# Performance work log

Measured on AMD Instinct MI355X. Metric: run time of the kernel, lower is better.

The kernel has to match this reference:

```python
import jax, jax.numpy as jnp
import numpy as np
import math

DIM = 2048
B = 4
L = 4096
LOCAL_WINDOW = 512
GLOBAL_STRIDE = 1024
TOTAL_SEEN = 65536


def _sparse_cache_positions(total_seen):
    # Positions kept by _build_sparse_cache: local window tail + global strided.
    local_start = max(0, total_seen - LOCAL_WINDOW)
    glob = np.arange(0, local_start, GLOBAL_STRIDE)
    loc = np.arange(local_start, total_seen)
    return np.concatenate([glob, loc]).astype(np.int64)  # sorted, 576 entries


def setup_inputs() -> dict:
    key = jax.random.key(0)
    ks = jax.random.split(key, 12)
    pos = _sparse_cache_positions(TOTAL_SEEN)
    Kc = pos.shape[0]  # 576
    inp = {
        "chunk": jax.random.normal(ks[0], (B, L, DIM), dtype=jnp.float32),
        "cached_k": jax.random.normal(ks[1], (B, Kc, DIM), dtype=jnp.float32),
        "cached_v": jax.random.normal(ks[2], (B, Kc, DIM), dtype=jnp.float32),
        "cached_positions": jnp.asarray(pos),
        "total_seen": TOTAL_SEEN,
        "Wq": jax.random.normal(ks[3], (DIM, DIM), dtype=jnp.float32) * 0.02,
        "bq": jnp.zeros((DIM,), dtype=jnp.float32),
        "Wk": jax.random.normal(ks[4], (DIM, DIM), dtype=jnp.float32) * 0.02,
        "bk": jnp.zeros((DIM,), dtype=jnp.float32),
        "Wv": jax.random.normal(ks[5], (DIM, DIM), dtype=jnp.float32) * 0.02,
        "bv": jnp.zeros((DIM,), dtype=jnp.float32),
        "Wo": jax.random.normal(ks[6], (DIM, DIM), dtype=jnp.float32) * 0.02,
        "bo": jnp.zeros((DIM,), dtype=jnp.float32),
    }
    return inp


def reference(chunk, cached_k, cached_v, cached_positions, total_seen,
              Wq, bq, Wk, bk, Wv, bv, Wo, bo):
    Bn, Ln, D = chunk.shape
    scale = 1.0 / math.sqrt(D)
    # QKV projections (nn.Linear: x @ W.T + b)
    q = chunk @ Wq.T + bq            # [B, L, D]
    new_k = chunk @ Wk.T + bk        # [B, L, D]
    new_v = chunk @ Wv.T + bv
    new_pos = jnp.arange(total_seen, total_seen + Ln)  # [L]
    full_k = jnp.concatenate([cached_k, new_k], axis=1)   # [B, Kc+L, D]
    full_v = jnp.concatenate([cached_v, new_v], axis=1)
    full_pos = jnp.concatenate([cached_positions, new_pos], axis=0)  # [Kc+L]
    # Masked dense attention (causal on absolute positions)
    scores = jnp.einsum('bqd,bkd->bqk', q, full_k) * scale  # [B, L, Kc+L]
    causal = full_pos[None, :] > new_pos[:, None]           # [L, Kc+L]
    scores = jnp.where(causal[None, :, :], -jnp.inf, scores)
    weights = jax.nn.softmax(scores, axis=-1)
    attended = jnp.einsum('bqk,bkd->bqd', weights, full_v)  # [B, L, D]
    return attended @ Wo.T + bo
```

## Files before the change

### kernel.cpp

```cpp
#include <hip/hip_runtime.h>
#include <hip/hip_bf16.h>
#include <hip/hip_fp16.h>
#include <math.h>

#define B_   4
#define L_   4096
#define D_   2048
#define KC_  576
#define KT_  4672
#define KTP_ 4736

typedef __attribute__((ext_vector_type(8))) short short8;
typedef __attribute__((ext_vector_type(4))) float floatx4;

enum { EPI_BF16 = 0, EPI_KV = 1, EPI_SCORE = 2, EPI_F32 = 3 };
enum { FLAG_SWZ = 1, FLAG_KCAP = 2 };

__device__ static inline void gl_lds16(const void* g, void* l) {
  __builtin_amdgcn_global_load_lds((const __attribute__((address_space(1))) void*)g,
                                   (__attribute__((address_space(3))) void*)l,
                                   16, 0, 0);
}

__global__ __launch_bounds__(256) void gemm_bt(
    const ushort* __restrict__ A, int lda,
    const ushort* __restrict__ Bt, int ldb,
    void* __restrict__ out, int ldo,
    const float* __restrict__ bias,
    int K, int mode, int flags, float scale)
{
  __shared__ __align__(16) ushort As[128 * 32];
  __shared__ __align__(16) ushort Bs[128 * 32];
  const int t    = threadIdx.x;
  const int lane = t & 63;
  const int wave = t >> 6;

  int m_idx, n_idx;
  if (flags & FLAG_SWZ) {
    const int bid = blockIdx.x + (gridDim.x * blockIdx.y);
    n_idx = 2 * (bid & 7) + ((bid >> 3) & 1);
    m_idx = bid >> 4;
  } else {
    n_idx = blockIdx.x;
    m_idx = blockIdx.y;
  }
  const int bm = m_idx * 128;
  const int bn = n_idx * 128;

  if (mode == EPI_SCORE && bn >= KC_ + bm + 128) return;
  if (flags & FLAG_KCAP) {
    const int kcap = 704 + 128 * m_idx;
    if (K > kcap) K = kcap;
  }

  const int wm = (wave & 1) * 64;
  const int wn = (wave >> 1) * 64;

  floatx4 acc[4][4];
#pragma unroll
  for (int i = 0; i < 4; i++)
#pragma unroll
    for (int j = 0; j < 4; j++) acc[i][j] = (floatx4)(0.0f);

  const int srow = t >> 2;
  const int scol = (t & 3) * 8;
  const ushort* Ag = A  + (size_t)(bm + srow) * lda + scol;
  const ushort* Bg = Bt + (size_t)(bn + srow) * ldb + scol;
  char* AsB = (char*)As + wave * 1024;
  char* BsB = (char*)Bs + wave * 1024;
  const int fr = lane & 15;
  const int fq = lane >> 4;

  for (int k0 = 0; k0 < K; k0 += 32) {
    __syncthreads();
    gl_lds16(Ag + k0,                        AsB);
    gl_lds16(Ag + (size_t)64 * lda + k0,     AsB + 4096);
    gl_lds16(Bg + k0,                        BsB);
    gl_lds16(Bg + (size_t)64 * ldb + k0,     BsB + 4096);
    __syncthreads();

    short8 af[4], bf[4];
#pragma unroll
    for (int i = 0; i < 4; i++)
      af[i] = *(const short8*)(As + (wm + i * 16 + fr) * 32 + fq * 8);
#pragma unroll
    for (int j = 0; j < 4; j++)
      bf[j] = *(const short8*)(Bs + (wn + j * 16 + fr) * 32 + fq * 8);
#pragma unroll
    for (int i = 0; i < 4; i++)
#pragma unroll
      for (int j = 0; j < 4; j++)
        acc[i][j] = __builtin_amdgcn_mfma_f32_16x16x32_bf16(af[i], bf[j], acc[i][j], 0, 0, 0);
  }

#pragma unroll
  for (int i = 0; i < 4; i++) {
#pragma unroll
    for (int j = 0; j < 4; j++) {
      const int col = bn + wn + j * 16 + fr;
#pragma unroll
      for (int r = 0; r < 4; r++) {
        const int row = bm + wm + i * 16 + fq * 4 + r;
        float v = acc[i][j][r];
        if (mode == EPI_SCORE) {
          v *= scale;
          bool masked = (col >= KT_) || (col >= KC_ && (col - KC_) > row);
          if (masked) v = -65504.0f;
          ((__half*)out)[(size_t)row * ldo + col] = __float2half(v);
        } else if (mode == EPI_F32) {
          if (bias) v += bias[col];
          ((float*)out)[(size_t)row * ldo + col] = v;
        } else if (mode == EPI_KV) {
          if (bias) v += bias[col];
          const int b = row >> 12;
          const int l = row & 4095;
          ((__hip_bfloat16*)out)[((size_t)b * KTP_ + KC_ + l) * D_ + col] = __float2bfloat16(v);
        } else {
          if (bias) v += bias[col];
          ((__hip_bfloat16*)out)[(size_t)row * ldo + col] = __float2bfloat16(v);
        }
      }
    }
  }
}

__global__ __launch_bounds__(256) void cvt_f32_bf16(const float* __restrict__ in,
                                                    __hip_bfloat16* __restrict__ out, int n) {
  int i = blockIdx.x * 256 + threadIdx.x;
  int stride = gridDim.x * 256;
  for (; i < n; i += stride) out[i] = __float2bfloat16(in[i]);
}

__global__ __launch_bounds__(256) void cvt_weights(const float* __restrict__ wq,
                                                   const float* __restrict__ wk,
                                                   const float* __restrict__ wv,
                                                   const float* __restrict__ wo,
                                                   __hip_bfloat16* __restrict__ out) {
  const int per = D_ * D_;
  const int n = 4 * per;
  int i = blockIdx.x * 256 + threadIdx.x;
  int stride = gridDim.x * 256;
  for (; i < n; i += stride) {
    int w = i / per, rem = i - w * per;
    const float* src = (w == 0) ? wq : (w == 1) ? wk : (w == 2) ? wv : wo;
    out[i] = __float2bfloat16(src[rem]);
  }
}

__global__ __launch_bounds__(256) void cvt_cached(const float* __restrict__ ck,
                                                  const float* __restrict__ cv,
                                                  ushort* __restrict__ fk,
                                                  ushort* __restrict__ fv) {
  const int n = B_ * KC_ * D_;
  int i = blockIdx.x * 256 + threadIdx.x;
  int stride = gridDim.x * 256;
  for (; i < n; i += stride) {
    int b = i / (KC_ * D_);
    int rem = i - b * (KC_ * D_);
    size_t o = (size_t)b * KTP_ * D_ + rem;
    __hip_bfloat16 k16 = __float2bfloat16(ck[i]);
    __hip_bfloat16 v16 = __float2bfloat16(cv[i]);
    fk[o] = *(ushort*)&k16;
    fv[o] = *(ushort*)&v16;
  }
}

__global__ __launch_bounds__(256) void zero_pad(ushort* __restrict__ fk, ushort* __restrict__ fv) {
  const int n = B_ * (KTP_ - KT_) * D_;
  int i = blockIdx.x * 256 + threadIdx.x;
  int stride = gridDim.x * 256;
  for (; i < n; i += stride) {
    int b = i / ((KTP_ - KT_) * D_);
    int rem = i - b * ((KTP_ - KT_) * D_);
    size_t o = (size_t)b * KTP_ * D_ + (size_t)KT_ * D_ + rem;
    fk[o] = 0;
    fv[o] = 0;
  }
}

__global__ __launch_bounds__(256) void transpose_k(const ushort* __restrict__ in,
                                                   ushort* __restrict__ out) {
  __shared__ ushort tile[32][33];
  const int bx = blockIdx.x * 32;
  const int by = blockIdx.y * 32;
  const int t = threadIdx.x;
  for (int e = t; e < 1024; e += 256) {
    int r = e >> 5, c = e & 31;
    tile[r][c] = in[(size_t)(bx + r) * D_ + by + c];
  }
  __syncthreads();
  for (int e = t; e < 1024; e += 256) {
    int r = e >> 5, c = e & 31;
    out[(size_t)(by + r) * KTP_ + bx + c] = tile[c][r];
  }
}

__global__ __launch_bounds__(256) void softmax_rows(ushort* __restrict__ Sbuf) {
  const int row = blockIdx.x;
  const int nvalid = KC_ + row + 1;
  const int wcap = 704 + (row & ~127);
  ushort* sr = Sbuf + (size_t)row * KTP_;
  const int t = threadIdx.x;
  float vals[19];
  float m = -1e30f;
  int nit = (wcap - t + 255) / 256;
#pragma unroll
  for (int i = 0; i < 19; i++) {
    int idx = i * 256 + t;
    float v = -1e30f;
    if (idx < nvalid) v = __half2float(((const __half*)sr)[idx]);
    vals[i] = v;
    m = fmaxf(m, v);
    if (i + 1 >= nit) break;
  }
  __shared__ float red[256];
  red[t] = m;
  __syncthreads();
  for (int s = 128; s > 0; s >>= 1) {
    if (t < s) red[t] = fmaxf(red[t], red[t + s]);
    __syncthreads();
  }
  m = red[0];
  __syncthreads();
  float sum = 0.0f;
#pragma unroll
  for (int i = 0; i < 19; i++) {
    int idx = i * 256 + t;
    if (idx < wcap) {
      float e = (idx < nvalid) ? __expf(vals[i] - m) : 0.0f;
      vals[i] = e;
      sum += e;
    }
    if (i + 1 >= nit) break;
  }
  red[t] = sum;
  __syncthreads();
  for (int s = 128; s > 0; s >>= 1) {
    if (t < s) red[t] += red[t + s];
    __syncthreads();
  }
  float inv = 1.0f / red[0];
#pragma unroll
  for (int i = 0; i < 19; i++) {
    int idx = i * 256 + t;
    if (idx < wcap) {
      __hip_bfloat16 w = __float2bfloat16(vals[i] * inv);
      sr[idx] = *(ushort*)&w;
    }
    if (i + 1 >= nit) break;
  }
}

extern "C" void kernel_launch(void* const* d_in, const int* in_sizes, int n_in,
                              void* d_out, int out_size, void* d_ws, size_t ws_size,
                              hipStream_t stream) {
  const float* chunk    = (const float*)d_in[0];
  const float* cached_k = (const float*)d_in[1];
  const float* cached_v = (const float*)d_in[2];
  const float* Wq = (const float*)d_in[5];
  const float* bq = (const float*)d_in[6];
  const float* Wk = (const float*)d_in[7];
  const float* bk = (const float*)d_in[8];
  const float* Wv = (const float*)d_in[9];
  const float* bv = (const float*)d_in[10];
  const float* Wo = (const float*)d_in[11];
  const float* bo = (const float*)d_in[12];
  float* out = (float*)d_out;

  char* ws = (char*)d_ws;
  size_t off = 0;
  auto alloc = [&](size_t bytes) -> char* {
    char* p = ws + off;
    off += (bytes + 255) & ~(size_t)255;
    return p;
  };
  ushort* wall = (ushort*)alloc((size_t)4 * D_ * D_ * 2);
  ushort* wqb = wall;
  ushort* wkb = wall + (size_t)D_ * D_;
  ushort* wvb = wall + (size_t)2 * D_ * D_;
  ushort* wob = wall + (size_t)3 * D_ * D_;
  ushort* cbf = (ushort*)alloc((size_t)B_ * L_ * D_ * 2);
  ushort* qbf = (ushort*)alloc((size_t)B_ * L_ * D_ * 2);
  ushort* fk  = (ushort*)alloc((size_t)B_ * KTP_ * D_ * 2);
  ushort* fv  = (ushort*)alloc((size_t)B_ * KTP_ * D_ * 2);
  ushort* Sb  = (ushort*)alloc((size_t)L_ * KTP_ * 2);
  ushort* vt  = (ushort*)alloc((size_t)D_ * KTP_ * 2);

  dim3 blk(256);

  cvt_f32_bf16<<<8192, blk, 0, stream>>>(chunk, (__hip_bfloat16*)cbf, B_ * L_ * D_);
  cvt_weights<<<4096, blk, 0, stream>>>(Wq, Wk, Wv, Wo, (__hip_bfloat16*)wall);
  cvt_cached<<<2048, blk, 0, stream>>>(cached_k, cached_v, fk, fv);
  zero_pad<<<512, blk, 0, stream>>>(fk, fv);

  gemm_bt<<<dim3(D_ / 128, (B_ * L_) / 128), blk, 0, stream>>>(
      cbf, D_, wqb, D_, qbf, D_, bq, D_, EPI_BF16, FLAG_SWZ, 1.0f);
  gemm_bt<<<dim3(D_ / 128, (B_ * L_) / 128), blk, 0, stream>>>(
      cbf, D_, wkb, D_, fk, D_, bk, D_, EPI_KV, FLAG_SWZ, 1.0f);
  gemm_bt<<<dim3(D_ / 128, (B_ * L_) / 128), blk, 0, stream>>>(
      cbf, D_, wvb, D_, fv, D_, bv, D_, EPI_KV, FLAG_SWZ, 1.0f);

  const float scale = 1.0f / sqrtf((float)D_);

  for (int b = 0; b < B_; b++) {
    const ushort* qb  = qbf + (size_t)b * L_ * D_;
    const ushort* fkb = fk  + (size_t)b * KTP_ * D_;
    const ushort* fvb = fv  + (size_t)b * KTP_ * D_;
    ushort* ab = cbf + (size_t)b * L_ * D_;

    transpose_k<<<dim3(KTP_ / 32, D_ / 32), blk, 0, stream>>>(fvb, vt);
    gemm_bt<<<dim3(KTP_ / 128, L_ / 128), blk, 0, stream>>>(
        qb, D_, fkb, D_, Sb, KTP_, nullptr, D_, EPI_SCORE, 0, scale);
    softmax_rows<<<L_, blk, 0, stream>>>(Sb);
    gemm_bt<<<dim3(D_ / 128, L_ / 128), blk, 0, stream>>>(
        Sb, KTP_, vt, KTP_, ab, D_, nullptr, KTP_, EPI_BF16, FLAG_SWZ | FLAG_KCAP, 1.0f);
  }

  gemm_bt<<<dim3(D_ / 128, (B_ * L_) / 128), blk, 0, stream>>>(
      cbf, D_, wob, D_, out, D_, bo, D_, EPI_F32, FLAG_SWZ, 1.0f);
}
```

Measured before the change: 2.156 ms.

## Rewrite GEMM as 256x256 tile, 8-wave double-buffered pipeline with swizzled LDS

The bf16 GEMM goes from 128x128 tiles with 4 waves and a single-buffered K=32 loop to 256x256 tiles with 8 waves. The new loop double-buffers K=64 stages in 128KB of LDS, interleaving async global-to-LDS loads with MFMA quarter-steps and raising priority around the MFMA blocks. LDS addresses use an XOR swizzle to avoid bank conflicts, and the block remapping becomes an XCD-aware chunked layout that is now also applied to the score GEMM. Padding, kcap and the softmax window are retuned to 256-row granularity, which adds some wasted masked work on the causal-triangle GEMMs.

```diff
diff --git a/kernel.cpp b/kernel.cpp
--- a/kernel.cpp
+++ b/kernel.cpp
@@ -8,7 +8,7 @@
 #define D_   2048
 #define KC_  576
 #define KT_  4672
-#define KTP_ 4736
+#define KTP_ 4864
 
 typedef __attribute__((ext_vector_type(8))) short short8;
 typedef __attribute__((ext_vector_type(4))) float floatx4;
@@ -22,86 +22,166 @@
                                    16, 0, 0);
 }
 
-__global__ __launch_bounds__(256) void gemm_bt(
+__device__ static inline void barx() {
+  asm volatile("" ::: "memory");
+  __builtin_amdgcn_s_barrier();
+  asm volatile("" ::: "memory");
+}
+
+__global__ __launch_bounds__(512, 2) void gemm_bt(
     const ushort* __restrict__ A, int lda,
     const ushort* __restrict__ Bt, int ldb,
     void* __restrict__ out, int ldo,
     const float* __restrict__ bias,
     int K, int mode, int flags, float scale)
 {
-  __shared__ __align__(16) ushort As[128 * 32];
-  __shared__ __align__(16) ushort Bs[128 * 32];
-  const int t    = threadIdx.x;
-  const int lane = t & 63;
-  const int wave = t >> 6;
+  __shared__ __align__(16) char smem[2 * 4 * 16384];
+
+  const int t = threadIdx.x;
+  const int l = t & 63;
+  const int wv = t >> 6;
 
   int m_idx, n_idx;
   if (flags & FLAG_SWZ) {
-    const int bid = blockIdx.x + (gridDim.x * blockIdx.y);
-    n_idx = 2 * (bid & 7) + ((bid >> 3) & 1);
-    m_idx = bid >> 4;
+    const int total = gridDim.x * gridDim.y;
+    const int chunk = total >> 3;
+    const int orig = blockIdx.y * gridDim.x + blockIdx.x;
+    const int wg = (orig & 7) * chunk + (orig >> 3);
+    m_idx = wg % gridDim.y;
+    n_idx = wg / gridDim.y;
   } else {
     n_idx = blockIdx.x;
     m_idx = blockIdx.y;
   }
-  const int bm = m_idx * 128;
-  const int bn = n_idx * 128;
-
-  if (mode == EPI_SCORE && bn >= KC_ + bm + 128) return;
+  const int bm = m_idx * 256;
+  const int bn = n_idx * 256;
+
+  if (mode == EPI_SCORE && bn >= KC_ + bm + 256) return;
   if (flags & FLAG_KCAP) {
-    const int kcap = 704 + 128 * m_idx;
+    const int kcap = 832 + 256 * m_idx;
     if (K > kcap) K = kcap;
   }
 
-  const int wm = (wave & 1) * 64;
-  const int wn = (wave >> 1) * 64;
-
-  floatx4 acc[4][4];
-#pragma unroll
-  for (int i = 0; i < 4; i++)
-#pragma unroll
-    for (int j = 0; j < 4; j++) acc[i][j] = (floatx4)(0.0f);
+  const int wr = wv >> 2, wc = wv & 3;
+  const int wm = wr << 7;
+  const int wcn = wc << 6;
+  const int fr = l & 15, fq = l >> 4;
+  const int swz = fq ^ ((l >> 1) & 3);
+
+  int offA[8], offB[4];
+#pragma unroll
+  for (int i = 0; i < 8; ++i) offA[i] = (wm + i * 16 + fr) * 64 + swz * 16;
+#pragma unroll
+  for (int j = 0; j < 4; ++j) offB[j] = (wcn + j * 16 + fr) * 64 + swz * 16;
 
   const int srow = t >> 2;
-  const int scol = (t & 3) * 8;
-  const ushort* Ag = A  + (size_t)(bm + srow) * lda + scol;
-  const ushort* Bg = Bt + (size_t)(bn + srow) * ldb + scol;
-  char* AsB = (char*)As + wave * 1024;
-  char* BsB = (char*)Bs + wave * 1024;
-  const int fr = lane & 15;
-  const int fq = lane >> 4;
-
-  for (int k0 = 0; k0 < K; k0 += 32) {
-    __syncthreads();
-    gl_lds16(Ag + k0,                        AsB);
-    gl_lds16(Ag + (size_t)64 * lda + k0,     AsB + 4096);
-    gl_lds16(Bg + k0,                        BsB);
-    gl_lds16(Bg + (size_t)64 * ldb + k0,     BsB + 4096);
-    __syncthreads();
-
-    short8 af[4], bf[4];
-#pragma unroll
-    for (int i = 0; i < 4; i++)
-      af[i] = *(const short8*)(As + (wm + i * 16 + fr) * 32 + fq * 8);
-#pragma unroll
-    for (int j = 0; j < 4; j++)
-      bf[j] = *(const short8*)(Bs + (wn + j * 16 + fr) * 32 + fq * 8);
-#pragma unroll
-    for (int i = 0; i < 4; i++)
-#pragma unroll
-      for (int j = 0; j < 4; j++)
-        acc[i][j] = __builtin_amdgcn_mfma_f32_16x16x32_bf16(af[i], bf[j], acc[i][j], 0, 0, 0);
-  }
-
-#pragma unroll
-  for (int i = 0; i < 4; i++) {
-#pragma unroll
-    for (int j = 0; j < 4; j++) {
-      const int col = bn + wn + j * 16 + fr;
-#pragma unroll
-      for (int r = 0; r < 4; r++) {
-        const int row = bm + wm + i * 16 + fq * 4 + r;
-        float v = acc[i][j][r];
+  const int sslot = (t & 3) ^ ((t >> 3) & 3);
+  const ushort* Ag = A + (size_t)(bm + srow) * lda + sslot * 8;
+  const ushort* Bg = Bt + (size_t)(bn + srow) * ldb + sslot * 8;
+  const int wofs = wv << 10;
+
+  auto stageA = [&](int d, int kh, int kt) {
+    char* dst = smem + (((d << 2) + kh) << 14) + wofs;
+    const ushort* g = Ag + kt + (kh << 5);
+    gl_lds16(g, dst);
+    gl_lds16(g + ((size_t)lda << 7), dst + 8192);
+  };
+  auto stageB = [&](int d, int kh, int kt) {
+    char* dst = smem + (((d << 2) + 2 + kh) << 14) + wofs;
+    const ushort* g = Bg + kt + (kh << 5);
+    gl_lds16(g, dst);
+    gl_lds16(g + ((size_t)ldb << 7), dst + 8192);
+  };
+
+  floatx4 acc[8][4];
+#pragma unroll
+  for (int i = 0; i < 8; ++i)
+#pragma unroll
+    for (int j = 0; j < 4; ++j) acc[i][j] = (floatx4)(0.0f);
+
+  const int nkt = K >> 6;
+  const int k1 = (nkt > 1) ? 64 : 0;
+
+  stageA(0, 0, 0); stageB(0, 0, 0);
+  stageA(0, 1, 0); stageB(0, 1, 0);
+  stageA(1, 0, k1); stageB(1, 0, k1);
+  asm volatile("s_waitcnt vmcnt(4)" ::: "memory");
+  barx();
+
+  for (int T = 0; T < nkt; ++T) {
+    const int cur = T & 1;
+    const char* rb = smem + (cur << 16);
+    const int kA = ((T + 1 < nkt) ? T + 1 : nkt - 1) << 6;
+    const int kB = ((T + 2 < nkt) ? T + 2 : nkt - 1) << 6;
+    short8 afr[4], bfr[4];
+
+#pragma unroll
+    for (int i = 0; i < 4; ++i) afr[i] = *(const short8*)(rb + offA[i]);
+#pragma unroll
+    for (int j = 0; j < 4; ++j) bfr[j] = *(const short8*)(rb + 32768 + offB[j]);
+    stageA(cur ^ 1, 1, kA);
+    barx();
+    __builtin_amdgcn_s_setprio(1);
+#pragma unroll
+    for (int i = 0; i < 4; ++i)
+#pragma unroll
+      for (int j = 0; j < 4; ++j)
+        acc[i][j] = __builtin_amdgcn_mfma_f32_16x16x32_bf16(afr[i], bfr[j], acc[i][j], 0, 0, 0);
+    __builtin_amdgcn_s_setprio(0);
+    barx();
+
+#pragma unroll
+    for (int i = 0; i < 4; ++i) afr[i] = *(const short8*)(rb + offA[4 + i]);
+    stageB(cur ^ 1, 1, kA);
+    barx();
+    __builtin_amdgcn_s_setprio(1);
+#pragma unroll
+    for (int i = 0; i < 4; ++i)
+#pragma unroll
+      for (int j = 0; j < 4; ++j)
+        acc[4 + i][j] = __builtin_amdgcn_mfma_f32_16x16x32_bf16(afr[i], bfr[j], acc[4 + i][j], 0, 0, 0);
+    __builtin_amdgcn_s_setprio(0);
+    barx();
+
+#pragma unroll
+    for (int i = 0; i < 4; ++i) afr[i] = *(const short8*)(rb + 16384 + offA[i]);
+#pragma unroll
+    for (int j = 0; j < 4; ++j) bfr[j] = *(const short8*)(rb + 49152 + offB[j]);
+    stageA(cur, 0, kB);
+    barx();
+    __builtin_amdgcn_s_setprio(1);
+#pragma unroll
+    for (int i = 0; i < 4; ++i)
+#pragma unroll
+      for (int j = 0; j < 4; ++j)
+        acc[i][j] = __builtin_amdgcn_mfma_f32_16x16x32_bf16(afr[i], bfr[j], acc[i][j], 0, 0, 0);
+    __builtin_amdgcn_s_setprio(0);
+    barx();
+
+#pragma unroll
+    for (int i = 0; i < 4; ++i) afr[i] = *(const short8*)(rb + 16384 + offA[4 + i]);
+    stageB(cur, 0, kB);
+    asm volatile("s_waitcnt vmcnt(4)" ::: "memory");
+    barx();
+    __builtin_amdgcn_s_setprio(1);
+#pragma unroll
+    for (int i = 0; i < 4; ++i)
+#pragma unroll
+      for (int j = 0; j < 4; ++j)
+        acc[4 + i][j] = __builtin_amdgcn_mfma_f32_16x16x32_bf16(afr[i], bfr[j], acc[4 + i][j], 0, 0, 0);
+    __builtin_amdgcn_s_setprio(0);
+    barx();
+  }
+
+#pragma unroll
+  for (int mf = 0; mf < 8; ++mf) {
+#pragma unroll
+    for (int nf = 0; nf < 4; ++nf) {
+      const int col = bn + wcn + nf * 16 + fr;
+#pragma unroll
+      for (int r = 0; r < 4; ++r) {
+        const int row = bm + wm + mf * 16 + fq * 4 + r;
+        float v = acc[mf][nf][r];
         if (mode == EPI_SCORE) {
           v *= scale;
           bool masked = (col >= KT_) || (col >= KC_ && (col - KC_) > row);
@@ -113,8 +193,8 @@
         } else if (mode == EPI_KV) {
           if (bias) v += bias[col];
           const int b = row >> 12;
-          const int l = row & 4095;
-          ((__hip_bfloat16*)out)[((size_t)b * KTP_ + KC_ + l) * D_ + col] = __float2bfloat16(v);
+          const int ll = row & 4095;
+          ((__hip_bfloat16*)out)[((size_t)b * KTP_ + KC_ + ll) * D_ + col] = __float2bfloat16(v);
         } else {
           if (bias) v += bias[col];
           ((__hip_bfloat16*)out)[(size_t)row * ldo + col] = __float2bfloat16(v);
@@ -198,7 +278,7 @@
 __global__ __launch_bounds__(256) void softmax_rows(ushort* __restrict__ Sbuf) {
   const int row = blockIdx.x;
   const int nvalid = KC_ + row + 1;
-  const int wcap = 704 + (row & ~127);
+  const int wcap = 832 + (row & ~255);
   ushort* sr = Sbuf + (size_t)row * KTP_;
   const int t = threadIdx.x;
   float vals[19];
@@ -287,17 +367,18 @@
   ushort* vt  = (ushort*)alloc((size_t)D_ * KTP_ * 2);
 
   dim3 blk(256);
+  dim3 gblk(512);
 
   cvt_f32_bf16<<<8192, blk, 0, stream>>>(chunk, (__hip_bfloat16*)cbf, B_ * L_ * D_);
   cvt_weights<<<4096, blk, 0, stream>>>(Wq, Wk, Wv, Wo, (__hip_bfloat16*)wall);
   cvt_cached<<<2048, blk, 0, stream>>>(cached_k, cached_v, fk, fv);
   zero_pad<<<512, blk, 0, stream>>>(fk, fv);
 
-  gemm_bt<<<dim3(D_ / 128, (B_ * L_) / 128), blk, 0, stream>>>(
+  gemm_bt<<<dim3(D_ / 256, (B_ * L_) / 256), gblk, 0, stream>>>(
       cbf, D_, wqb, D_, qbf, D_, bq, D_, EPI_BF16, FLAG_SWZ, 1.0f);
-  gemm_bt<<<dim3(D_ / 128, (B_ * L_) / 128), blk, 0, stream>>>(
+  gemm_bt<<<dim3(D_ / 256, (B_ * L_) / 256), gblk, 0, stream>>>(
       cbf, D_, wkb, D_, fk, D_, bk, D_, EPI_KV, FLAG_SWZ, 1.0f);
-  gemm_bt<<<dim3(D_ / 128, (B_ * L_) / 128), blk, 0, stream>>>(
+  gemm_bt<<<dim3(D_ / 256, (B_ * L_) / 256), gblk, 0, stream>>>(
       cbf, D_, wvb, D_, fv, D_, bv, D_, EPI_KV, FLAG_SWZ, 1.0f);
 
   const float scale = 1.0f / sqrtf((float)D_);
@@ -309,13 +390,13 @@
     ushort* ab = cbf + (size_t)b * L_ * D_;
 
     transpose_k<<<dim3(KTP_ / 32, D_ / 32), blk, 0, stream>>>(fvb, vt);
-    gemm_bt<<<dim3(KTP_ / 128, L_ / 128), blk, 0, stream>>>(
-        qb, D_, fkb, D_, Sb, KTP_, nullptr, D_, EPI_SCORE, 0, scale);
+    gemm_bt<<<dim3(KTP_ / 256, L_ / 256), gblk, 0, stream>>>(
+        qb, D_, fkb, D_, Sb, KTP_, nullptr, D_, EPI_SCORE, FLAG_SWZ, scale);
     softmax_rows<<<L_, blk, 0, stream>>>(Sb);
-    gemm_bt<<<dim3(D_ / 128, L_ / 128), blk, 0, stream>>>(
-        Sb, KTP_, vt, KTP_, ab, D_, nullptr, KTP_, EPI_BF16, FLAG_SWZ | FLAG_KCAP, 1.0f);
-  }
-
-  gemm_bt<<<dim3(D_ / 128, (B_ * L_) / 128), blk, 0, stream>>>(
+    gemm_bt<<<dim3(D_ / 256, L_ / 256), gblk, 0, stream>>>(
+        Sb, KTP_, vt, KTP_, ab, D_, nullptr, KT_, EPI_BF16, FLAG_SWZ | FLAG_KCAP, 1.0f);
+  }
+
+  gemm_bt<<<dim3(D_ / 256, (B_ * L_) / 256), gblk, 0, stream>>>(
       cbf, D_, wob, D_, out, D_, bo, D_, EPI_F32, FLAG_SWZ, 1.0f);
 }
```

Result: faster. 2.050 ms (-4.9%).
